# Kernel tuning notes

Measured on AMD Instinct MI355X. Metric: run time of the kernel, lower is better.

The kernel has to match this reference:

```python
import jax, jax.numpy as jnp
import numpy as np

N = 100000      # nodes
E = 1000000     # edges
IN = 512
H = [512, 256]
C = 64          # n_classes
K = 10          # propagation steps
ALPHA = 0.1


def _glorot(key, shape):
    lim = np.sqrt(6.0 / (shape[0] + shape[1])).astype(np.float32)
    return jax.random.uniform(key, shape, jnp.float32, -lim, lim)


def setup_inputs() -> dict:
    key = jax.random.key(0)
    ks = jax.random.split(key, 6)
    features = jax.random.normal(ks[0], (N, IN), jnp.float32)
    edge_index = jax.random.randint(ks[1], (2, E), 0, N)  # int32/64 src,dst
    W0 = _glorot(ks[2], (H[0], IN)); b0 = jnp.zeros((H[0],), jnp.float32)
    W1 = _glorot(ks[3], (H[1], H[0])); b1 = jnp.zeros((H[1],), jnp.float32)
    W2 = _glorot(ks[4], (C, H[1])); b2 = jnp.zeros((C,), jnp.float32)
    return dict(features=features, edge_index=edge_index,
                W0=W0, b0=b0, W1=W1, b1=b1, W2=W2, b2=b2)


def _appnp(h, src, dst):
    # DGL APPNPConv: symmetric normalization D_out^{-1/2} A D_in^{-1/2},
    # degrees clamped to min 1; h_{t+1} = (1-a) * norm_agg + a * h_0.
    ones = jnp.ones(src.shape, h.dtype)
    deg_out = jax.ops.segment_sum(ones, src, num_segments=N)
    deg_in = jax.ops.segment_sum(ones, dst, num_segments=N)
    norm_src = jnp.maximum(deg_out, 1.0) ** -0.5  # [N]
    norm_dst = jnp.maximum(deg_in, 1.0) ** -0.5   # [N]
    h0 = h
    for _ in range(K):
        msg = (h * norm_src[:, None])[src]                     # [E, C] gather
        agg = jax.ops.segment_sum(msg, dst, num_segments=N)    # [N, C] scatter-add
        h = (1.0 - ALPHA) * agg * norm_dst[:, None] + ALPHA * h0
    return h


def reference(features, edge_index, W0, b0, W1, b1, W2, b2):
    src, dst = edge_index[0], edge_index[1]
    h = jax.nn.relu(features @ W0.T + b0)   # [N, 512]
    h = jax.nn.relu(h @ W1.T + b1)          # [N, 256]
    h = h @ W2.T + b2                       # [N, 64] logits
    return _appnp(h, src, dst)
```

## Files before the change

kernel.cpp:

```cpp
#include <hip/hip_runtime.h>
#include <hip/hip_bf16.h>

#define NN_NODES 100000
#define NE_EDGES 1000000
#define D_IN 512
#define D_H0 512
#define D_H1 256
#define D_C  64

using f32x4  = __attribute__((ext_vector_type(4))) float;
using h16x8  = __attribute__((ext_vector_type(8))) _Float16;

static __device__ __forceinline__ void gll16(const _Float16* g, _Float16* l){
    __builtin_amdgcn_global_load_lds(
        (const __attribute__((address_space(1))) unsigned int*)g,
        (__attribute__((address_space(3))) unsigned int*)l, 16, 0, 0);
}

__global__ __launch_bounds__(256) void tof16_tiled_kernel(
    const float* __restrict__ w, _Float16* __restrict__ o, int R, int K)
{
    int i = blockIdx.x * 256 + threadIdx.x;
    int n8 = R * (K >> 3);
    if (i >= n8) return;
    int kd = K >> 3;
    int r  = i / kd;
    int c0 = (i - r * kd) * 8;
    const f32x4 a = *(const f32x4*)(w + (size_t)r * K + c0);
    const f32x4 b = *(const f32x4*)(w + (size_t)r * K + c0 + 4);
    h16x8 h;
    #pragma unroll
    for (int j = 0; j < 4; j++){
        h[j]   = (_Float16)a[j];
        h[j+4] = (_Float16)b[j];
    }
    size_t off = ((size_t)(r >> 7) * (K >> 5) + (c0 >> 5)) * 4096
               + (size_t)(r & 127) * 32 + (c0 & 31);
    *(h16x8*)(o + off) = h;
}

template<bool RELU, int OMODE, int BN_T, int NBN, int KK>
__global__ __launch_bounds__(256, 4) void gemm_kernel(
    const _Float16* __restrict__ A,
    const _Float16* __restrict__ B,
    const float* __restrict__ bias,
    void* __restrict__ O1, _Float16* __restrict__ O2, const float* __restrict__ scale,
    int M, int NNc, int xq, int xr)
{
    constexpr int NTK  = KK / 32;
    constexpr int NF   = BN_T / 32;
    constexpr int BBLK = BN_T / 16;
    constexpr int TOT  = 8 + BBLK;
    constexpr int LPW  = TOT / 4;

    __shared__ _Float16 sA[2][128 * 32];
    __shared__ _Float16 sB[2][BN_T * 32];

    const int tid  = threadIdx.x;
    const int lane = tid & 63;
    const int wv   = tid >> 6;
    const int wm   = wv >> 1;
    const int wn   = wv & 1;
    const int fr   = lane & 15;
    const int fc   = lane >> 4;

    const int bid = blockIdx.x;
    const int xcd = bid & 7;
    const int i8  = bid >> 3;
    const int L   = ((xcd < xr) ? xcd * (xq + 1) : xr * (xq + 1) + (xcd - xr) * xq) + i8;
    const int mt  = L / NBN;
    const int bn  = L - mt * NBN;
    const int bm0 = mt * 128;
    const int bn0 = bn * BN_T;

    const int bslab = bn0 >> 7;
    const int binsl = bn0 & 127;

    const int loff = (lane >> 2) * 32 + ((lane & 3) ^ ((lane >> 3) & 3)) * 8;

    f32x4 acc[4][NF] = {};

    auto stage = [&](int b, int t){
        const _Float16* as = A + ((size_t)mt * NTK + t) * 4096;
        const _Float16* bs = B + ((size_t)bslab * NTK + t) * 4096 + binsl * 32;
        #pragma unroll
        for (int u = 0; u < LPW; u++){
            int idx = u * 4 + wv;
            if (idx < 8) gll16(as + idx * 512 + loff, sA[b] + idx * 512);
            else         gll16(bs + (idx - 8) * 512 + loff, sB[b] + (idx - 8) * 512);
        }
    };

    auto compute = [&](int b){
        h16x8 bf[NF];
        #pragma unroll
        for (int nf = 0; nf < NF; nf++){
            int r = wn * (BN_T / 2) + nf * 16 + fr;
            int c = (fc ^ ((r >> 1) & 3)) * 8;
            bf[nf] = *(const h16x8*)&sB[b][r * 32 + c];
        }
        h16x8 af[4];
        #pragma unroll
        for (int mf = 0; mf < 4; mf++){
            int r = wm * 64 + mf * 16 + fr;
            int c = (fc ^ ((r >> 1) & 3)) * 8;
            af[mf] = *(const h16x8*)&sA[b][r * 32 + c];
        }
        __builtin_amdgcn_s_setprio(1);
        #pragma unroll
        for (int mf = 0; mf < 4; mf++)
            #pragma unroll
            for (int nf = 0; nf < NF; nf++)
                acc[mf][nf] = __builtin_amdgcn_mfma_f32_16x16x32_f16(af[mf], bf[nf], acc[mf][nf], 0, 0, 0);
        __builtin_amdgcn_s_setprio(0);
    };

    stage(0, 0);
    __syncthreads();
    int cur = 0;
    for (int t = 0; t < NTK; t++){
        if (t + 1 < NTK) stage(cur ^ 1, t + 1);
        compute(cur);
        __syncthreads();
        cur ^= 1;
    }

    #pragma unroll
    for (int mf = 0; mf < 4; mf++){
        #pragma unroll
        for (int nf = 0; nf < NF; nf++){
            #pragma unroll
            for (int r = 0; r < 4; r++){
                int rg = bm0 + wm * 64 + mf * 16 + fc * 4 + r;
                int cg = bn0 + wn * (BN_T / 2) + nf * 16 + fr;
                if (rg < M){
                    float v = acc[mf][nf][r] + bias[cg];
                    if constexpr (RELU) v = fmaxf(v, 0.f);
                    if constexpr (OMODE == 1){
                        size_t o = ((size_t)mt * (NNc >> 5) + (cg >> 5)) * 4096
                                 + (size_t)(rg & 127) * 32 + (cg & 31);
                        ((_Float16*)O1)[o] = (_Float16)v;
                    } else {
                        ((_Float16*)O1)[(size_t)rg * NNc + cg] = (_Float16)v;
                        O2[(size_t)rg * NNc + cg] = (_Float16)(v * scale[rg]);
                    }
                }
            }
        }
    }
}

__global__ void degrees_kernel(const int* __restrict__ src, const int* __restrict__ dst,
                               int* __restrict__ dout, int* __restrict__ din){
    int e = blockIdx.x * blockDim.x + threadIdx.x;
    if (e < NE_EDGES){
        atomicAdd(&dout[src[e]], 1);
        atomicAdd(&din[dst[e]], 1);
    }
}

__global__ void norm_kernel(const int* __restrict__ dout, const int* __restrict__ din,
                            float* __restrict__ ns, float* __restrict__ nd, int n){
    int i = blockIdx.x * blockDim.x + threadIdx.x;
    if (i < n){
        ns[i] = rsqrtf((float)(dout[i] > 1 ? dout[i] : 1));
        nd[i] = rsqrtf((float)(din[i]  > 1 ? din[i]  : 1));
    }
}

__global__ __launch_bounds__(256) void scan1_kernel(const int* __restrict__ din,
                                                    int* __restrict__ part,
                                                    int* __restrict__ bsum, int n){
    __shared__ int s[256];
    int i = blockIdx.x * 256 + threadIdx.x;
    int v = (i < n) ? din[i] : 0;
    s[threadIdx.x] = v;
    __syncthreads();
    for (int off = 1; off < 256; off <<= 1){
        int t = (threadIdx.x >= off) ? s[threadIdx.x - off] : 0;
        __syncthreads();
        s[threadIdx.x] += t;
        __syncthreads();
    }
    if (i < n) part[i] = s[threadIdx.x];
    if (threadIdx.x == 255) bsum[blockIdx.x] = s[255];
}

__global__ __launch_bounds__(512) void scan2_kernel(int* __restrict__ bsum, int nb){
    __shared__ int s[512];
    int v = (threadIdx.x < nb) ? bsum[threadIdx.x] : 0;
    s[threadIdx.x] = v;
    __syncthreads();
    for (int off = 1; off < 512; off <<= 1){
        int t = (threadIdx.x >= off) ? s[threadIdx.x - off] : 0;
        __syncthreads();
        s[threadIdx.x] += t;
        __syncthreads();
    }
    if (threadIdx.x < nb) bsum[threadIdx.x] = s[threadIdx.x];
}

__global__ void scan3_kernel(const int* __restrict__ part, const int* __restrict__ din,
                             const int* __restrict__ bsum, int* __restrict__ offs,
                             int* __restrict__ cur, int n){
    int i = blockIdx.x * 256 + threadIdx.x;
    if (i < n){
        int base = (blockIdx.x > 0) ? bsum[blockIdx.x - 1] : 0;
        int excl = base + part[i] - din[i];
        offs[i] = excl;
        cur[i]  = excl;
    }
}

__global__ void fill_kernel(const int* __restrict__ src, const int* __restrict__ dst,
                            int* __restrict__ cur, int* __restrict__ csr){
    int e = blockIdx.x * blockDim.x + threadIdx.x;
    if (e < NE_EDGES){
        int d = dst[e];
        int pos = atomicAdd(&cur[d], 1);
        csr[pos] = src[e];
    }
}

__global__ __launch_bounds__(256) void propagate_kernel(
    const _Float16* __restrict__ hs, const _Float16* __restrict__ h0h,
    float* __restrict__ hout, _Float16* __restrict__ houts,
    const int* __restrict__ offs, const int* __restrict__ din,
    const int* __restrict__ csr,
    const float* __restrict__ ns, const float* __restrict__ nd)
{
    int t    = blockIdx.x * 256 + threadIdx.x;
    int node = t >> 3;
    int gl   = t & 7;
    if (node >= NN_NODES) return;
    int start = offs[node];
    int deg   = din[node];
    float acc[8] = {};
    int j = 0;
    for (; j + 2 <= deg; j += 2){
        int s0 = csr[start + j];
        int s1 = csr[start + j + 1];
        h16x8 v0 = *(const h16x8*)(hs + (size_t)s0 * D_C + gl * 8);
        h16x8 v1 = *(const h16x8*)(hs + (size_t)s1 * D_C + gl * 8);
        #pragma unroll
        for (int i = 0; i < 8; i++) acc[i] += (float)v0[i] + (float)v1[i];
    }
    if (j < deg){
        int s0 = csr[start + j];
        h16x8 v0 = *(const h16x8*)(hs + (size_t)s0 * D_C + gl * 8);
        #pragma unroll
        for (int i = 0; i < 8; i++) acc[i] += (float)v0[i];
    }
    float ndv = 0.9f * nd[node];
    h16x8 h0v = *(const h16x8*)(h0h + (size_t)node * D_C + gl * 8);
    float out[8];
    #pragma unroll
    for (int i = 0; i < 8; i++) out[i] = acc[i] * ndv + 0.1f * (float)h0v[i];
    if (houts){
        float nsv = ns[node];
        h16x8 o;
        #pragma unroll
        for (int i = 0; i < 8; i++) o[i] = (_Float16)(out[i] * nsv);
        *(h16x8*)(houts + (size_t)node * D_C + gl * 8) = o;
    }
    if (hout){
        f32x4 oa, ob;
        #pragma unroll
        for (int i = 0; i < 4; i++){ oa[i] = out[i]; ob[i] = out[i + 4]; }
        *(f32x4*)(hout + (size_t)node * D_C + gl * 8)     = oa;
        *(f32x4*)(hout + (size_t)node * D_C + gl * 8 + 4) = ob;
    }
}

extern "C" void kernel_launch(void* const* d_in, const int* in_sizes, int n_in,
                              void* d_out, int out_size, void* d_ws, size_t ws_size,
                              hipStream_t stream)
{
    const float* features = (const float*)d_in[0];
    const int*   edge     = (const int*)d_in[1];
    const float* W0 = (const float*)d_in[2];
    const float* b0 = (const float*)d_in[3];
    const float* W1 = (const float*)d_in[4];
    const float* b1 = (const float*)d_in[5];
    const float* W2 = (const float*)d_in[6];
    const float* b2 = (const float*)d_in[7];
    const int* src = edge;
    const int* dst = edge + NE_EDGES;

    char* p = (char*)d_ws;
    auto alloc = [&](size_t bytes) -> char* {
        char* r = p;
        p += (bytes + 255) & ~(size_t)255;
        return r;
    };

    const int MT = (NN_NODES + 127) / 128;
    const size_t FEAT_T = (size_t)MT * 16 * 4096 * 2;
    const size_t HBUFH  = (size_t)NN_NODES * D_C * 2;

    _Float16* w0f = (_Float16*)alloc((size_t)4 * 16 * 4096 * 2);
    _Float16* w1f = (_Float16*)alloc((size_t)2 * 16 * 4096 * 2);
    _Float16* w2f = (_Float16*)alloc((size_t)1 * 8  * 4096 * 2);
    char* R1 = alloc(FEAT_T);
    char* R2 = alloc(FEAT_T);
    int*   deg_out = (int*)alloc((size_t)NN_NODES * 4);
    int*   deg_in  = (int*)alloc((size_t)NN_NODES * 4);
    float* nsrc    = (float*)alloc((size_t)NN_NODES * 4);
    float* ndst    = (float*)alloc((size_t)NN_NODES * 4);
    int*   part    = (int*)alloc((size_t)NN_NODES * 4);
    int*   bsum    = (int*)alloc(2048);
    int*   offs    = (int*)alloc((size_t)NN_NODES * 4);
    int*   cur     = (int*)alloc((size_t)NN_NODES * 4);
    int*   csr     = (int*)alloc((size_t)NE_EDGES * 4);
    if ((size_t)(p - (char*)d_ws) > ws_size) return;

    _Float16* fhf  = (_Float16*)R1;
    _Float16* act2 = (_Float16*)R1;
    _Float16* act1 = (_Float16*)R2;
    _Float16* h0h  = (_Float16*)R2;
    _Float16* h0s  = (_Float16*)(R2 + HBUFH);
    _Float16* hAs  = (_Float16*)(R2 + 2 * HBUFH);
    _Float16* hBs  = (_Float16*)(R2 + 3 * HBUFH);

    hipMemsetAsync(deg_out, 0, (size_t)NN_NODES * 4, stream);
    hipMemsetAsync(deg_in,  0, (size_t)NN_NODES * 4, stream);
    degrees_kernel<<<(NE_EDGES + 255) / 256, 256, 0, stream>>>(src, dst, deg_out, deg_in);
    norm_kernel<<<(NN_NODES + 255) / 256, 256, 0, stream>>>(deg_out, deg_in, nsrc, ndst, NN_NODES);
    int nb = (NN_NODES + 255) / 256;
    scan1_kernel<<<nb, 256, 0, stream>>>(deg_in, part, bsum, NN_NODES);
    scan2_kernel<<<1, 512, 0, stream>>>(bsum, nb);
    scan3_kernel<<<nb, 256, 0, stream>>>(part, deg_in, bsum, offs, cur, NN_NODES);
    fill_kernel<<<(NE_EDGES + 255) / 256, 256, 0, stream>>>(src, dst, cur, csr);

    tof16_tiled_kernel<<<(NN_NODES * D_IN / 8 + 255) / 256, 256, 0, stream>>>(
        features, fhf, NN_NODES, D_IN);
    tof16_tiled_kernel<<<(D_H0 * D_IN / 8 + 255) / 256, 256, 0, stream>>>(W0, w0f, D_H0, D_IN);
    tof16_tiled_kernel<<<(D_H1 * D_H0 / 8 + 255) / 256, 256, 0, stream>>>(W1, w1f, D_H1, D_H0);
    tof16_tiled_kernel<<<(D_C * D_H1 / 8 + 255) / 256, 256, 0, stream>>>(W2, w2f, D_C, D_H1);

    {
        int nwg = MT * 8;
        gemm_kernel<true, 1, 64, 8, 512><<<nwg, 256, 0, stream>>>(
            fhf, w0f, b0, act1, nullptr, nullptr, NN_NODES, D_H0, nwg / 8, nwg % 8);
    }
    {
        int nwg = MT * 4;
        gemm_kernel<true, 1, 64, 4, 512><<<nwg, 256, 0, stream>>>(
            act1, w1f, b1, act2, nullptr, nullptr, NN_NODES, D_H1, nwg / 8, nwg % 8);
    }
    {
        int nwg = MT;
        gemm_kernel<false, 2, 64, 1, 256><<<nwg, 256, 0, stream>>>(
            act2, w2f, b2, h0h, h0s, nsrc, NN_NODES, D_C, nwg / 8, nwg % 8);
    }

    const _Float16* curs = h0s;
    _Float16* bufss[2] = { hAs, hBs };
    int pb = (NN_NODES * 8 + 255) / 256;
    for (int it = 0; it < 10; it++){
        float*    out  = (it == 9) ? (float*)d_out : nullptr;
        _Float16* outs = (it == 9) ? nullptr       : bufss[it & 1];
        propagate_kernel<<<pb, 256, 0, stream>>>(curs, h0h, out, outs, offs, deg_in, csr, nsrc, ndst);
        curs = outs;
    }
}
```

Measured before the change: 635.9 us.

## Load GEMM fragments directly from global memory into registers; unroll propagation gather by four

The GEMM kernel no longer stages A/B tiles through LDS with global_load_lds and barriers. Each wave now reads its MFMA fragments straight from the pre-tiled global buffers into registers, double-buffered in registers across k-steps. This removes LDS traffic and __syncthreads, but tiles shared between waves are fetched redundantly from global/L2, and the uncoalesced 16-byte loads can raise latency. The propagation kernel also unrolls its neighbor gather from 2 to 4 edges per iteration to expose more memory-level parallelism.

```diff
diff --git a/kernel.cpp b/kernel.cpp
--- a/kernel.cpp
+++ b/kernel.cpp
@@ -10,12 +10,6 @@
 
 using f32x4  = __attribute__((ext_vector_type(4))) float;
 using h16x8  = __attribute__((ext_vector_type(8))) _Float16;
-
-static __device__ __forceinline__ void gll16(const _Float16* g, _Float16* l){
-    __builtin_amdgcn_global_load_lds(
-        (const __attribute__((address_space(1))) unsigned int*)g,
-        (__attribute__((address_space(3))) unsigned int*)l, 16, 0, 0);
-}
 
 __global__ __launch_bounds__(256) void tof16_tiled_kernel(
     const float* __restrict__ w, _Float16* __restrict__ o, int R, int K)
@@ -47,14 +41,8 @@
     void* __restrict__ O1, _Float16* __restrict__ O2, const float* __restrict__ scale,
     int M, int NNc, int xq, int xr)
 {
-    constexpr int NTK  = KK / 32;
-    constexpr int NF   = BN_T / 32;
-    constexpr int BBLK = BN_T / 16;
-    constexpr int TOT  = 8 + BBLK;
-    constexpr int LPW  = TOT / 4;
-
-    __shared__ _Float16 sA[2][128 * 32];
-    __shared__ _Float16 sB[2][BN_T * 32];
+    constexpr int NTK = KK / 32;
+    constexpr int NF  = BN_T / 32;
 
     const int tid  = threadIdx.x;
     const int lane = tid & 63;
@@ -76,36 +64,30 @@
     const int bslab = bn0 >> 7;
     const int binsl = bn0 & 127;
 
-    const int loff = (lane >> 2) * 32 + ((lane & 3) ^ ((lane >> 3) & 3)) * 8;
+    int aoff[4], boff[NF];
+    #pragma unroll
+    for (int mf = 0; mf < 4; mf++)
+        aoff[mf] = (wm * 64 + mf * 16 + fr) * 32 + fc * 8;
+    #pragma unroll
+    for (int nf = 0; nf < NF; nf++)
+        boff[nf] = (binsl + wn * (BN_T / 2) + nf * 16 + fr) * 32 + fc * 8;
+
+    const _Float16* Abase = A + (size_t)mt * NTK * 4096;
+    const _Float16* Bbase = B + (size_t)bslab * NTK * 4096;
 
     f32x4 acc[4][NF] = {};
-
-    auto stage = [&](int b, int t){
-        const _Float16* as = A + ((size_t)mt * NTK + t) * 4096;
-        const _Float16* bs = B + ((size_t)bslab * NTK + t) * 4096 + binsl * 32;
-        #pragma unroll
-        for (int u = 0; u < LPW; u++){
-            int idx = u * 4 + wv;
-            if (idx < 8) gll16(as + idx * 512 + loff, sA[b] + idx * 512);
-            else         gll16(bs + (idx - 8) * 512 + loff, sB[b] + (idx - 8) * 512);
-        }
+    h16x8 a0[4], a1[4], b0[NF], b1[NF];
+
+    auto loadAB = [&](h16x8 (&af)[4], h16x8 (&bf)[NF], int t){
+        const _Float16* as = Abase + t * 4096;
+        const _Float16* bs = Bbase + t * 4096;
+        #pragma unroll
+        for (int mf = 0; mf < 4; mf++) af[mf] = *(const h16x8*)(as + aoff[mf]);
+        #pragma unroll
+        for (int nf = 0; nf < NF; nf++) bf[nf] = *(const h16x8*)(bs + boff[nf]);
     };
 
-    auto compute = [&](int b){
-        h16x8 bf[NF];
-        #pragma unroll
-        for (int nf = 0; nf < NF; nf++){
-            int r = wn * (BN_T / 2) + nf * 16 + fr;
-            int c = (fc ^ ((r >> 1) & 3)) * 8;
-            bf[nf] = *(const h16x8*)&sB[b][r * 32 + c];
-        }
-        h16x8 af[4];
-        #pragma unroll
-        for (int mf = 0; mf < 4; mf++){
-            int r = wm * 64 + mf * 16 + fr;
-            int c = (fc ^ ((r >> 1) & 3)) * 8;
-            af[mf] = *(const h16x8*)&sA[b][r * 32 + c];
-        }
+    auto mma = [&](h16x8 (&af)[4], h16x8 (&bf)[NF]){
         __builtin_amdgcn_s_setprio(1);
         #pragma unroll
         for (int mf = 0; mf < 4; mf++)
@@ -115,15 +97,17 @@
         __builtin_amdgcn_s_setprio(0);
     };
 
-    stage(0, 0);
-    __syncthreads();
-    int cur = 0;
-    for (int t = 0; t < NTK; t++){
-        if (t + 1 < NTK) stage(cur ^ 1, t + 1);
-        compute(cur);
-        __syncthreads();
-        cur ^= 1;
-    }
+    loadAB(a0, b0, 0);
+    #pragma unroll
+    for (int t = 0; t < NTK - 2; t += 2){
+        loadAB(a1, b1, t + 1);
+        mma(a0, b0);
+        loadAB(a0, b0, t + 2);
+        mma(a1, b1);
+    }
+    loadAB(a1, b1, NTK - 1);
+    mma(a0, b0);
+    mma(a1, b1);
 
     #pragma unroll
     for (int mf = 0; mf < 4; mf++){
@@ -237,15 +221,20 @@
     int deg   = din[node];
     float acc[8] = {};
     int j = 0;
-    for (; j + 2 <= deg; j += 2){
+    for (; j + 4 <= deg; j += 4){
         int s0 = csr[start + j];
         int s1 = csr[start + j + 1];
+        int s2 = csr[start + j + 2];
+        int s3 = csr[start + j + 3];
         h16x8 v0 = *(const h16x8*)(hs + (size_t)s0 * D_C + gl * 8);
         h16x8 v1 = *(const h16x8*)(hs + (size_t)s1 * D_C + gl * 8);
-        #pragma unroll
-        for (int i = 0; i < 8; i++) acc[i] += (float)v0[i] + (float)v1[i];
-    }
-    if (j < deg){
+        h16x8 v2 = *(const h16x8*)(hs + (size_t)s2 * D_C + gl * 8);
+        h16x8 v3 = *(const h16x8*)(hs + (size_t)s3 * D_C + gl * 8);
+        #pragma unroll
+        for (int i = 0; i < 8; i++)
+            acc[i] += ((float)v0[i] + (float)v1[i]) + ((float)v2[i] + (float)v3[i]);
+    }
+    for (; j < deg; j++){
         int s0 = csr[start + j];
         h16x8 v0 = *(const h16x8*)(hs + (size_t)s0 * D_C + gl * 8);
         #pragma unroll
```

Measured after the change: 714.2 us. +12.3%, slower.

## Triple-buffer GEMM LDS staging with explicit vmcnt waits; unroll propagation gather by four

Applied to the files above, without the earlier changes.

The GEMM main loop moves from double to triple buffering of the A/B tiles in shared memory. It prefetches two K-steps ahead and uses manual s_waitcnt vmcnt plus raw s_barrier in place of __syncthreads, so global-to-LDS loads overlap more with MFMA compute. Separately, the propagation gather loop is unrolled to four neighbors per iteration to expose more memory-level parallelism. The cost is more LDS per block, which may reduce occupancy under launch_bounds(256,4). The hard-coded vmcnt counts also assume an exact number of loads per stage, so a mismatch could cause races.

```diff
diff --git a/kernel.cpp b/kernel.cpp
--- a/kernel.cpp
+++ b/kernel.cpp
@@ -53,8 +53,8 @@
     constexpr int TOT  = 8 + BBLK;
     constexpr int LPW  = TOT / 4;
 
-    __shared__ _Float16 sA[2][128 * 32];
-    __shared__ _Float16 sB[2][BN_T * 32];
+    __shared__ _Float16 sA[3][128 * 32];
+    __shared__ _Float16 sB[3][BN_T * 32];
 
     const int tid  = threadIdx.x;
     const int lane = tid & 63;
@@ -116,13 +116,22 @@
     };
 
     stage(0, 0);
-    __syncthreads();
-    int cur = 0;
+    stage(1, 1);
     for (int t = 0; t < NTK; t++){
-        if (t + 1 < NTK) stage(cur ^ 1, t + 1);
-        compute(cur);
-        __syncthreads();
-        cur ^= 1;
+        if (t + 2 < NTK){
+            stage((t + 2) % 3, t + 2);
+            asm volatile("s_waitcnt vmcnt(6)" ::: "memory");
+        } else if (t + 1 < NTK){
+            asm volatile("s_waitcnt vmcnt(3)" ::: "memory");
+        } else {
+            asm volatile("s_waitcnt vmcnt(0)" ::: "memory");
+        }
+        __builtin_amdgcn_s_barrier();
+        asm volatile("" ::: "memory");
+        compute(t % 3);
+        asm volatile("" ::: "memory");
+        __builtin_amdgcn_s_barrier();
+        asm volatile("" ::: "memory");
     }
 
     #pragma unroll
@@ -237,15 +246,20 @@
     int deg   = din[node];
     float acc[8] = {};
     int j = 0;
-    for (; j + 2 <= deg; j += 2){
+    for (; j + 4 <= deg; j += 4){
         int s0 = csr[start + j];
         int s1 = csr[start + j + 1];
+        int s2 = csr[start + j + 2];
+        int s3 = csr[start + j + 3];
         h16x8 v0 = *(const h16x8*)(hs + (size_t)s0 * D_C + gl * 8);
         h16x8 v1 = *(const h16x8*)(hs + (size_t)s1 * D_C + gl * 8);
-        #pragma unroll
-        for (int i = 0; i < 8; i++) acc[i] += (float)v0[i] + (float)v1[i];
-    }
-    if (j < deg){
+        h16x8 v2 = *(const h16x8*)(hs + (size_t)s2 * D_C + gl * 8);
+        h16x8 v3 = *(const h16x8*)(hs + (size_t)s3 * D_C + gl * 8);
+        #pragma unroll
+        for (int i = 0; i < 8; i++)
+            acc[i] += ((float)v0[i] + (float)v1[i]) + ((float)v2[i] + (float)v3[i]);
+    }
+    for (; j < deg; j++){
         int s0 = csr[start + j];
         h16x8 v0 = *(const h16x8*)(hs + (size_t)s0 * D_C + gl * 8);
         #pragma unroll
```

Measured after the change: 639.5 us. About the same (+0.6%).

## Fuse second and third GEMM layers into one kernel; unroll gather by four

Applied to the files above, without the earlier changes.

Adds a fused kernel that computes the 256-wide hidden layer for a 128-row tile, keeps the ReLU output in shared memory in swizzled form, and immediately multiplies it by the 64-column final weight. This removes the round trip of the layer-2 activation through global memory and one kernel launch. The propagation gather loop is also unrolled to four neighbours per iteration to expose more memory-level parallelism. The fused kernel uses 512 threads and 96KB of shared memory, which may limit occupancy, and buffer aliasing is reassigned so the propagation buffers sit in R1.

```diff
diff --git a/kernel.cpp b/kernel.cpp
--- a/kernel.cpp
+++ b/kernel.cpp
@@ -150,6 +150,144 @@
     }
 }
 
+__global__ __launch_bounds__(512, 2) void gemm23_kernel(
+    const _Float16* __restrict__ A,
+    const _Float16* __restrict__ B1,
+    const _Float16* __restrict__ B2,
+    const float* __restrict__ bias1,
+    const float* __restrict__ bias2,
+    _Float16* __restrict__ h0h, _Float16* __restrict__ h0s,
+    const float* __restrict__ nsrc,
+    int M, int xq, int xr)
+{
+    constexpr int NTK = 16;
+    __shared__ _Float16 smem[49152];
+
+    const int tid  = threadIdx.x;
+    const int lane = tid & 63;
+    const int wv   = tid >> 6;
+    const int wm   = wv >> 2;
+    const int wn   = wv & 3;
+    const int fr   = lane & 15;
+    const int fc   = lane >> 4;
+
+    const int bid = blockIdx.x;
+    const int xcd = bid & 7;
+    const int i8  = bid >> 3;
+    const int mt  = ((xcd < xr) ? xcd * (xq + 1) : xr * (xq + 1) + (xcd - xr) * xq) + i8;
+    const int bm0 = mt * 128;
+
+    const int loff = (lane >> 2) * 32 + ((lane & 3) ^ ((lane >> 3) & 3)) * 8;
+
+    _Float16* sW2 = smem + 32768;
+
+    #pragma unroll
+    for (int u = 0; u < 4; u++){
+        int idx = u * 8 + wv;
+        int k = idx >> 2, rb = idx & 3;
+        gll16(B2 + (size_t)k * 4096 + rb * 512 + loff, sW2 + k * 2048 + rb * 512);
+    }
+
+    auto sA = [&](int b){ return smem + b * 12288; };
+    auto sB = [&](int b){ return smem + b * 12288 + 4096; };
+
+    auto stage = [&](int b, int t){
+        #pragma unroll
+        for (int u = 0; u < 3; u++){
+            int idx = u * 8 + wv;
+            if (idx < 8){
+                gll16(A + ((size_t)mt * NTK + t) * 4096 + idx * 512 + loff,
+                      sA(b) + idx * 512);
+            } else {
+                int rb = idx - 8;
+                gll16(B1 + ((size_t)(rb >> 3) * NTK + t) * 4096 + (rb & 7) * 512 + loff,
+                      sB(b) + rb * 512);
+            }
+        }
+    };
+
+    f32x4 acc[4][4] = {};
+
+    auto compute = [&](int b){
+        h16x8 bf[4];
+        #pragma unroll
+        for (int nf = 0; nf < 4; nf++){
+            int r = wn * 64 + nf * 16 + fr;
+            int c = (fc ^ ((r >> 1) & 3)) * 8;
+            bf[nf] = *(const h16x8*)&sB(b)[r * 32 + c];
+        }
+        h16x8 af[4];
+        #pragma unroll
+        for (int mf = 0; mf < 4; mf++){
+            int r = wm * 64 + mf * 16 + fr;
+            int c = (fc ^ ((r >> 1) & 3)) * 8;
+            af[mf] = *(const h16x8*)&sA(b)[r * 32 + c];
+        }
+        __builtin_amdgcn_s_setprio(1);
+        #pragma unroll
+        for (int mf = 0; mf < 4; mf++)
+            #pragma unroll
+            for (int nf = 0; nf < 4; nf++)
+                acc[mf][nf] = __builtin_amdgcn_mfma_f32_16x16x32_f16(af[mf], bf[nf], acc[mf][nf], 0, 0, 0);
+        __builtin_amdgcn_s_setprio(0);
+    };
+
+    stage(0, 0);
+    __syncthreads();
+    int cur = 0;
+    for (int t = 0; t < NTK; t++){
+        if (t + 1 < NTK) stage(cur ^ 1, t + 1);
+        compute(cur);
+        __syncthreads();
+        cur ^= 1;
+    }
+
+    #pragma unroll
+    for (int mf = 0; mf < 4; mf++){
+        #pragma unroll
+        for (int nf = 0; nf < 4; nf++){
+            #pragma unroll
+            for (int r = 0; r < 4; r++){
+                int row = wm * 64 + mf * 16 + fc * 4 + r;
+                int col = wn * 64 + nf * 16 + fr;
+                float v = fmaxf(acc[mf][nf][r] + bias1[col], 0.f);
+                int ci = col & 31;
+                int sw = ((ci >> 3) ^ ((row >> 1) & 3)) * 8 + (ci & 7);
+                smem[(col >> 5) * 4096 + row * 32 + sw] = (_Float16)v;
+            }
+        }
+    }
+    __syncthreads();
+
+    f32x4 acc2[4] = {};
+    #pragma unroll
+    for (int kk = 0; kk < 8; kk++){
+        int ar = wv * 16 + fr;
+        int ac = (fc ^ ((ar >> 1) & 3)) * 8;
+        h16x8 af = *(const h16x8*)&smem[kk * 4096 + ar * 32 + ac];
+        #pragma unroll
+        for (int nf = 0; nf < 4; nf++){
+            int br = nf * 16 + fr;
+            int bc = (fc ^ ((br >> 1) & 3)) * 8;
+            h16x8 bf = *(const h16x8*)&sW2[kk * 2048 + br * 32 + bc];
+            acc2[nf] = __builtin_amdgcn_mfma_f32_16x16x32_f16(af, bf, acc2[nf], 0, 0, 0);
+        }
+    }
+    #pragma unroll
+    for (int nf = 0; nf < 4; nf++){
+        #pragma unroll
+        for (int r = 0; r < 4; r++){
+            int rg = bm0 + wv * 16 + fc * 4 + r;
+            int cg = nf * 16 + fr;
+            if (rg < M){
+                float v = acc2[nf][r] + bias2[cg];
+                h0h[(size_t)rg * D_C + cg] = (_Float16)v;
+                h0s[(size_t)rg * D_C + cg] = (_Float16)(v * nsrc[rg]);
+            }
+        }
+    }
+}
+
 __global__ void degrees_kernel(const int* __restrict__ src, const int* __restrict__ dst,
                                int* __restrict__ dout, int* __restrict__ din){
     int e = blockIdx.x * blockDim.x + threadIdx.x;
@@ -237,15 +375,20 @@
     int deg   = din[node];
     float acc[8] = {};
     int j = 0;
-    for (; j + 2 <= deg; j += 2){
+    for (; j + 4 <= deg; j += 4){
         int s0 = csr[start + j];
         int s1 = csr[start + j + 1];
+        int s2 = csr[start + j + 2];
+        int s3 = csr[start + j + 3];
         h16x8 v0 = *(const h16x8*)(hs + (size_t)s0 * D_C + gl * 8);
         h16x8 v1 = *(const h16x8*)(hs + (size_t)s1 * D_C + gl * 8);
-        #pragma unroll
-        for (int i = 0; i < 8; i++) acc[i] += (float)v0[i] + (float)v1[i];
-    }
-    if (j < deg){
+        h16x8 v2 = *(const h16x8*)(hs + (size_t)s2 * D_C + gl * 8);
+        h16x8 v3 = *(const h16x8*)(hs + (size_t)s3 * D_C + gl * 8);
+        #pragma unroll
+        for (int i = 0; i < 8; i++)
+            acc[i] += ((float)v0[i] + (float)v1[i]) + ((float)v2[i] + (float)v3[i]);
+    }
+    for (; j < deg; j++){
         int s0 = csr[start + j];
         h16x8 v0 = *(const h16x8*)(hs + (size_t)s0 * D_C + gl * 8);
         #pragma unroll
@@ -315,12 +458,11 @@
     if ((size_t)(p - (char*)d_ws) > ws_size) return;
 
     _Float16* fhf  = (_Float16*)R1;
-    _Float16* act2 = (_Float16*)R1;
     _Float16* act1 = (_Float16*)R2;
-    _Float16* h0h  = (_Float16*)R2;
-    _Float16* h0s  = (_Float16*)(R2 + HBUFH);
-    _Float16* hAs  = (_Float16*)(R2 + 2 * HBUFH);
-    _Float16* hBs  = (_Float16*)(R2 + 3 * HBUFH);
+    _Float16* h0h  = (_Float16*)R1;
+    _Float16* h0s  = (_Float16*)(R1 + HBUFH);
+    _Float16* hAs  = (_Float16*)(R1 + 2 * HBUFH);
+    _Float16* hBs  = (_Float16*)(R1 + 3 * HBUFH);
 
     hipMemsetAsync(deg_out, 0, (size_t)NN_NODES * 4, stream);
     hipMemsetAsync(deg_in,  0, (size_t)NN_NODES * 4, stream);
@@ -344,14 +486,9 @@
             fhf, w0f, b0, act1, nullptr, nullptr, NN_NODES, D_H0, nwg / 8, nwg % 8);
     }
     {
-        int nwg = MT * 4;
-        gemm_kernel<true, 1, 64, 4, 512><<<nwg, 256, 0, stream>>>(
-            act1, w1f, b1, act2, nullptr, nullptr, NN_NODES, D_H1, nwg / 8, nwg % 8);
-    }
-    {
         int nwg = MT;
-        gemm_kernel<false, 2, 64, 1, 256><<<nwg, 256, 0, stream>>>(
-            act2, w2f, b2, h0h, h0s, nsrc, NN_NODES, D_C, nwg / 8, nwg % 8);
+        gemm23_kernel<<<nwg, 512, 0, stream>>>(
+            act1, w1f, w2f, b1, b2, h0h, h0s, nsrc, NN_NODES, nwg / 8, nwg % 8);
     }
 
     const _Float16* curs = h0s;
```

Result: faster. 609.0 us (-4.2%).
